# Kernel optimization log

Measured on AMD Instinct MI355X. Metric: run time of the kernel, lower is better.

Reference implementation:

```python
import jax, jax.numpy as jnp
import numpy as np

B_, L_, H_, N_ = 8, 1024, 1024, 64

def setup_inputs() -> dict:
    key = jax.random.key(0)
    k1, k2, k3, k4 = jax.random.split(key, 4)
    return {
        "samples": jax.random.normal(k1, (B_, L_, 3 * H_), dtype=jnp.float32),
        "label_one_hot": jax.random.uniform(k2, (B_, L_, N_), dtype=jnp.float32),
        "predict": jax.random.normal(k3, (B_, L_, N_), dtype=jnp.float32),
        "W": jax.random.normal(k4, (H_, 3 * H_), dtype=jnp.float32) * (1.0 / np.sqrt(3 * H_)),
        "b_proj": jnp.zeros((H_,), dtype=jnp.float32),
    }

def reference(samples, label_one_hot, predict, W, b_proj):
    # projection: Linear(3H -> H)
    s = jnp.einsum("blk,hk->blh", samples, W) + b_proj          # [b,L,H]
    # dense similarity graph with diagonal masked out, row-softmax
    graph = jnp.einsum("blh,bmh->blm", s, s)                     # [b,L,L]
    L = graph.shape[1]
    eye = jnp.eye(L, dtype=graph.dtype)
    A = jax.nn.softmax(graph - 1e5 * eye, axis=-1)               # [b,L,L]
    # centered masked labels
    sup = label_one_hot
    row_has = (jnp.sum(sup, axis=-1) > 0.5).astype(sup.dtype)    # [b,L]
    total = jnp.sum(row_has, axis=-1)[:, None]                   # [b,1]
    avg = (jnp.sum(sup, axis=-2) / total)[:, None, :]            # [b,1,N]
    B0 = (sup - avg) * row_has[..., None]                        # [b,L,N]
    # diagonal inverse-degree scaling (elementwise, no dense diag matmul)
    d = 1.0 / (jnp.sum(A, axis=-1) + 1e-10)                      # [b,L]
    P = d[:, :, None] * jnp.swapaxes(A, -1, -2)                  # [b,L,L]
    Db = d[:, :, None] * B0                                      # [b,L,N]
    # 6-step power-iteration scan with residual injection at t==3
    ut = jnp.zeros_like(B0)
    for t in range(1, 7):
        ut = jnp.einsum("blm,bmn->bln", P, ut) + Db
        if t == 3:
            ut = ut + predict  # dropout is identity in eval mode
    return ut

if __name__ == "__main__":
    out = reference(**setup_inputs())
    print(out.shape, out.dtype)
```

## Files before the change

kernel.cpp:

```cpp
#include <hip/hip_runtime.h>


typedef _Float16 f16_t;
typedef f16_t f16x4 __attribute__((ext_vector_type(4)));
typedef f16_t f16x8 __attribute__((ext_vector_type(8)));
typedef float floatx4 __attribute__((ext_vector_type(4)));

__device__ __forceinline__ void async_copy16(const void* g, void* l) {
  __builtin_amdgcn_global_load_lds(
      (const __attribute__((address_space(1))) void*)g,
      (__attribute__((address_space(3))) void*)l, 16, 0, 0);
}

__device__ __forceinline__ f16_t hi_of(float x) { return (f16_t)x; }
__device__ __forceinline__ f16_t lo_of(float x, f16_t h) {
  return (f16_t)(x - (float)h);
}

__global__ __launch_bounds__(256) void prep_kernel(
    const float* __restrict__ W, f16_t* __restrict__ Whi, f16_t* __restrict__ Wlo,
    const float* __restrict__ samples, f16_t* __restrict__ SampH)
{
  const int bx = blockIdx.x, tid = threadIdx.x;
  if (bx < 3072) {
    const int i = bx * 256 + tid;
    float4 v = ((const float4*)W)[i];
    v.x *= 32.f; v.y *= 32.f; v.z *= 32.f; v.w *= 32.f;
    f16x4 h, l;
    f16_t h0 = hi_of(v.x); h[0] = h0; l[0] = lo_of(v.x, h0);
    f16_t h1 = hi_of(v.y); h[1] = h1; l[1] = lo_of(v.y, h1);
    f16_t h2 = hi_of(v.z); h[2] = h2; l[2] = lo_of(v.z, h2);
    f16_t h3 = hi_of(v.w); h[3] = h3; l[3] = lo_of(v.w, h3);
    *(f16x4*)(Whi + (size_t)i * 4) = h;
    *(f16x4*)(Wlo + (size_t)i * 4) = l;
  } else {
    const int i = (bx - 3072) * 256 + tid;
    const float4 v = ((const float4*)samples)[i];
    f16x4 h;
    h[0] = (f16_t)v.x; h[1] = (f16_t)v.y; h[2] = (f16_t)v.z; h[3] = (f16_t)v.w;
    *(f16x4*)(SampH + (size_t)i * 4) = h;
  }
}

__global__ __launch_bounds__(512, 2) void gemm1_8ph(
    const f16_t* __restrict__ Ag,
    const f16_t* __restrict__ BhG, const f16_t* __restrict__ BlG,
    const float* __restrict__ bias,
    f16_t* __restrict__ Chi, f16_t* __restrict__ Clo,
    int N, int K, float cscale)
{
  __shared__ __align__(16) char smem[131072];

  const int tid = threadIdx.x;
  const int lane = tid & 63;
  const int wave = tid >> 6;
  const int wm = wave >> 2;
  const int wn = wave & 3;
  const int m0 = blockIdx.y * 256;
  const int n0 = blockIdx.x * 128;
  const int fr = lane & 15;
  const int lch = lane >> 4;

  const int gA0 = tid;
  const int gA1 = tid + 512;
  const int rA0 = gA0 >> 2, lcA0 = (gA0 & 3) ^ (rA0 & 3);
  const int rA1 = gA1 >> 2, lcA1 = (gA1 & 3) ^ (rA1 & 3);
  const int rB = tid >> 2, lcB = (tid & 3) ^ (rB & 3);
  const f16_t* aSrc0 = Ag + (size_t)(m0 + rA0) * K + lcA0 * 8;
  const f16_t* aSrc1 = Ag + (size_t)(m0 + rA1) * K + lcA1 * 8;
  const f16_t* bhSrc = BhG + (size_t)(n0 + rB) * K + lcB * 8;
  const f16_t* blSrc = BlG + (size_t)(n0 + rB) * K + lcB * 8;
  char* ldsA0 = smem + gA0 * 16;
  char* ldsA1 = smem + gA1 * 16;
  char* ldsBh = smem + 16384 + (size_t)tid * 16;
  char* ldsBl = smem + 24576 + (size_t)tid * 16;

  const int swz = ((lch ^ (fr & 3)) * 16);
  const int aoff = (wm * 128 + fr) * 64 + swz;
  const int boff = (wn * 32 + fr) * 64 + swz;

  floatx4 acc[8][2] = {};

#pragma unroll
  for (int s = 0; s < 3; ++s) {
    const int slot = s * 32768;
    const int k0 = s * 32;
    async_copy16(aSrc0 + k0, ldsA0 + slot);
    async_copy16(aSrc1 + k0, ldsA1 + slot);
    async_copy16(bhSrc + k0, ldsBh + slot);
    async_copy16(blSrc + k0, ldsBl + slot);
  }

  const int NS = K >> 5;
  for (int s = 0; s < NS; ++s) {
    asm volatile("s_waitcnt vmcnt(8)" ::: "memory");
    __builtin_amdgcn_s_barrier();

    const char* base = smem + (s & 3) * 32768;

    f16x8 bh0 = *(const f16x8*)(base + 16384 + boff);
    f16x8 bh1 = *(const f16x8*)(base + 16384 + boff + 1024);
    f16x8 bl0 = *(const f16x8*)(base + 24576 + boff);
    f16x8 bl1 = *(const f16x8*)(base + 24576 + boff + 1024);
    f16x8 a0[4];
#pragma unroll
    for (int i = 0; i < 4; ++i) a0[i] = *(const f16x8*)(base + aoff + i * 1024);

    {
      int ss = s + 3; if (ss >= NS) ss -= NS;
      const int slot = (ss & 3) * 32768;
      const int k0 = ss * 32;
      async_copy16(aSrc0 + k0, ldsA0 + slot);
      async_copy16(aSrc1 + k0, ldsA1 + slot);
      async_copy16(bhSrc + k0, ldsBh + slot);
      async_copy16(blSrc + k0, ldsBl + slot);
    }

    __builtin_amdgcn_s_setprio(1);
#pragma unroll
    for (int i = 0; i < 4; ++i) {
      acc[i][0] = __builtin_amdgcn_mfma_f32_16x16x32_f16(a0[i], bh0, acc[i][0], 0, 0, 0);
      acc[i][1] = __builtin_amdgcn_mfma_f32_16x16x32_f16(a0[i], bh1, acc[i][1], 0, 0, 0);
      acc[i][0] = __builtin_amdgcn_mfma_f32_16x16x32_f16(a0[i], bl0, acc[i][0], 0, 0, 0);
      acc[i][1] = __builtin_amdgcn_mfma_f32_16x16x32_f16(a0[i], bl1, acc[i][1], 0, 0, 0);
    }
    __builtin_amdgcn_s_setprio(0);

    f16x8 a1[4];
#pragma unroll
    for (int i = 0; i < 4; ++i) a1[i] = *(const f16x8*)(base + aoff + 4096 + i * 1024);

    __builtin_amdgcn_s_setprio(1);
#pragma unroll
    for (int i = 0; i < 4; ++i) {
      acc[i + 4][0] = __builtin_amdgcn_mfma_f32_16x16x32_f16(a1[i], bh0, acc[i + 4][0], 0, 0, 0);
      acc[i + 4][1] = __builtin_amdgcn_mfma_f32_16x16x32_f16(a1[i], bh1, acc[i + 4][1], 0, 0, 0);
      acc[i + 4][0] = __builtin_amdgcn_mfma_f32_16x16x32_f16(a1[i], bl0, acc[i + 4][0], 0, 0, 0);
      acc[i + 4][1] = __builtin_amdgcn_mfma_f32_16x16x32_f16(a1[i], bl1, acc[i + 4][1], 0, 0, 0);
    }
    __builtin_amdgcn_s_setprio(0);
  }
  asm volatile("s_waitcnt vmcnt(0)" ::: "memory");

  const int mr = (lane >> 4) * 4;
#pragma unroll
  for (int j = 0; j < 2; ++j) {
    const int n = n0 + wn * 32 + j * 16 + fr;
    const float bj = bias[n];
#pragma unroll
    for (int i = 0; i < 8; ++i) {
#pragma unroll
      for (int r = 0; r < 4; ++r) {
        const int m = m0 + wm * 128 + i * 16 + mr + r;
        float v = acc[i][j][r] * cscale + bj;
        f16_t h = hi_of(v);
        Chi[(size_t)m * N + n] = h;
        Clo[(size_t)m * N + n] = lo_of(v, h);
      }
    }
  }
}

template <int CMODE>
__global__ __launch_bounds__(256) void gemm_mfma(
    const f16_t* __restrict__ AhiG,
    const f16_t* __restrict__ BhiG, const f16_t* __restrict__ BloG,
    const float* __restrict__ bias,
    float* __restrict__ Cf, f16_t* __restrict__ Chi, f16_t* __restrict__ Clo,
    int M, int N, int K, long long sA, long long sB, long long sC, float cscale)
{
  AhiG += (long long)blockIdx.z * sA;
  BhiG += (long long)blockIdx.z * sB;
  BloG += (long long)blockIdx.z * sB;
  if (CMODE == 1) Cf += (long long)blockIdx.z * sC;

  __shared__ __align__(16) char smem[49152];
  f16_t* AsHi = (f16_t*)smem;
  f16_t* BsHi = (f16_t*)(smem + 16384);
  f16_t* BsLo = (f16_t*)(smem + 32768);

  const int tid = threadIdx.x;
  const int lane = tid & 63;
  const int wave = tid >> 6;
  const int wm = wave >> 1, wn = wave & 1;

  int m0, n0;
  if (CMODE == 0) {
    m0 = blockIdx.y * 128;
    n0 = blockIdx.x * 128;
  } else {
    int idx = blockIdx.x, i = 0, accu = 0;
    while (accu + i + 1 <= idx) { accu += i + 1; ++i; }
    m0 = i * 128;
    n0 = (idx - accu) * 128;
  }

  const int fr = lane & 15;
  const int kg = (lane >> 4) * 8;
  const int aoff = (wm * 64 + fr) * 32 + kg;
  const int boff = (wn * 64 + fr) * 32 + kg;

  floatx4 acc[4][4] = {};

  for (int k0 = 0; k0 < K; k0 += 64) {
    __syncthreads();
#pragma unroll
    for (int it = 0; it < 4; ++it) {
      const int cb = it * 256 + wave * 64;
      const int c = cb + lane;
      const int kk = c >> 9;
      const int row = (c >> 2) & 127;
      const int kc = kk * 32 + (c & 3) * 8;
      const size_t ga = (size_t)(m0 + row) * K + k0 + kc;
      const size_t gb = (size_t)(n0 + row) * K + k0 + kc;
      async_copy16(AhiG + ga, (char*)AsHi + (size_t)cb * 16);
      async_copy16(BhiG + gb, (char*)BsHi + (size_t)cb * 16);
      async_copy16(BloG + gb, (char*)BsLo + (size_t)cb * 16);
    }
    __syncthreads();

#pragma unroll
    for (int kk = 0; kk < 2; ++kk) {
      f16x8 ah[4], bh[4], bl[4];
#pragma unroll
      for (int t = 0; t < 4; ++t) {
        ah[t] = *(const f16x8*)&AsHi[kk * 4096 + aoff + t * 512];
        bh[t] = *(const f16x8*)&BsHi[kk * 4096 + boff + t * 512];
        bl[t] = *(const f16x8*)&BsLo[kk * 4096 + boff + t * 512];
      }
#pragma unroll
      for (int i = 0; i < 4; ++i)
#pragma unroll
        for (int j = 0; j < 4; ++j) {
          acc[i][j] = __builtin_amdgcn_mfma_f32_16x16x32_f16(ah[i], bh[j], acc[i][j], 0, 0, 0);
          acc[i][j] = __builtin_amdgcn_mfma_f32_16x16x32_f16(ah[i], bl[j], acc[i][j], 0, 0, 0);
        }
    }
  }

  const int mr = (lane >> 4) * 4;
#pragma unroll
  for (int j = 0; j < 4; ++j) {
    const int n = n0 + wn * 64 + j * 16 + fr;
    const float bj = (CMODE == 0) ? bias[n] : 0.f;
#pragma unroll
    for (int i = 0; i < 4; ++i) {
#pragma unroll
      for (int r = 0; r < 4; ++r) {
        const int m = m0 + wm * 64 + i * 16 + mr + r;
        float v = acc[i][j][r];
        if (CMODE == 0) {
          v = v * cscale + bj;
          f16_t h = hi_of(v);
          Chi[(size_t)m * N + n] = h;
          Clo[(size_t)m * N + n] = lo_of(v, h);
        } else {
          if (m == n) v -= 1e5f;
          Cf[(size_t)m * N + n] = v;
        }
      }
    }
  }

  if (CMODE == 1 && m0 != n0) {
    float* T = (float*)smem;
#pragma unroll
    for (int mc = 0; mc < 4; ++mc) {
      __syncthreads();
      if (wm == (mc >> 1)) {
        const int ibase = (mc & 1) * 2;
#pragma unroll
        for (int di = 0; di < 2; ++di) {
#pragma unroll
          for (int j = 0; j < 4; ++j) {
            const int nl = wn * 64 + j * 16 + fr;
#pragma unroll
            for (int r = 0; r < 4; ++r) {
              const int mloc = di * 16 + mr + r;
              T[nl * 36 + mloc] = acc[ibase + di][j][r];
            }
          }
        }
      }
      __syncthreads();
      const int row = tid >> 1, half = tid & 1;
      const float* src = &T[row * 36 + half * 16];
      float* dst = Cf + (size_t)(n0 + row) * N + m0 + mc * 32 + half * 16;
#pragma unroll
      for (int q = 0; q < 16; ++q) dst[q] = src[q];
    }
  }
}

__global__ __launch_bounds__(256) void rowstats_kernel(
    const float* __restrict__ G, float* __restrict__ mx, float* __restrict__ inv)
{
  __shared__ float red[4];
  const int tid = threadIdx.x;
  const float* g = G + (size_t)blockIdx.x * 1024;
  const float4 v = ((const float4*)g)[tid];

  float m = fmaxf(fmaxf(v.x, v.y), fmaxf(v.z, v.w));
#pragma unroll
  for (int off = 32; off > 0; off >>= 1) m = fmaxf(m, __shfl_down(m, off));
  if ((tid & 63) == 0) red[tid >> 6] = m;
  __syncthreads();
  m = fmaxf(fmaxf(red[0], red[1]), fmaxf(red[2], red[3]));
  __syncthreads();

  float s = __expf(v.x - m) + __expf(v.y - m) + __expf(v.z - m) + __expf(v.w - m);
#pragma unroll
  for (int off = 32; off > 0; off >>= 1) s += __shfl_down(s, off);
  if ((tid & 63) == 0) red[tid >> 6] = s;
  __syncthreads();
  if (tid == 0) {
    mx[blockIdx.x] = m;
    inv[blockIdx.x] = 1.0f / (red[0] + red[1] + red[2] + red[3]);
  }
}

__global__ __launch_bounds__(256) void make_at_kernel(
    const float* __restrict__ G, const float* __restrict__ mx,
    const float* __restrict__ inv, f16_t* __restrict__ At)
{
  const int row = blockIdx.x;
  const int b = row >> 10;
  const int tid = threadIdx.x;
  const float4 g = ((const float4*)(G + (size_t)row * 1024))[tid];
  const float4 m = ((const float4*)(mx + b * 1024))[tid];
  const float4 iv = ((const float4*)(inv + b * 1024))[tid];
  f16x4 o;
  o[0] = (f16_t)(__expf(g.x - m.x) * iv.x);
  o[1] = (f16_t)(__expf(g.y - m.y) * iv.y);
  o[2] = (f16_t)(__expf(g.z - m.z) * iv.z);
  o[3] = (f16_t)(__expf(g.w - m.w) * iv.w);
  *(f16x4*)(At + (size_t)row * 1024 + tid * 4) = o;
}

__global__ __launch_bounds__(1024) void make_db_kernel(
    const float* __restrict__ sup, float* __restrict__ Db, f16_t* __restrict__ DbT)
{
  const int L = 1024, Nn = 64;
  const float* s = sup + (size_t)blockIdx.x * L * Nn;
  float* db = Db + (size_t)blockIdx.x * L * Nn;
  f16_t* dbt = DbT + (size_t)blockIdx.x * L * Nn;
  __shared__ float rowhas[1024];
  __shared__ float cpart[1024];
  __shared__ float tpart[16];
  __shared__ float avg[64];
  __shared__ float totalsh;
  const int tid = threadIdx.x;

  const float4* sr = (const float4*)(s + (size_t)tid * 64);
  float ss = 0.f;
#pragma unroll
  for (int i = 0; i < 16; ++i) { const float4 v = sr[i]; ss += (v.x + v.y) + (v.z + v.w); }
  const float rh = (ss > 0.5f) ? 1.f : 0.f;
  rowhas[tid] = rh;
  float t = rh;
#pragma unroll
  for (int off = 32; off > 0; off >>= 1) t += __shfl_down(t, off);
  if ((tid & 63) == 0) tpart[tid >> 6] = t;

  const int n = tid & 63, seg = tid >> 6;
  float cs = 0.f;
  for (int l = seg * 64; l < seg * 64 + 64; ++l) cs += s[(size_t)l * 64 + n];
  cpart[seg * 64 + n] = cs;
  __syncthreads();
  if (tid == 0) { float tt = 0.f; for (int i = 0; i < 16; ++i) tt += tpart[i]; totalsh = tt; }
  __syncthreads();
  if (tid < 64) {
    float a = 0.f;
    for (int i = 0; i < 16; ++i) a += cpart[i * 64 + tid];
    avg[tid] = a / totalsh;
  }
  __syncthreads();

  const float4* s4 = (const float4*)s;
  float4* d4 = (float4*)db;
  for (int i = tid; i < (L * Nn) / 4; i += 1024) {
    float4 v = s4[i];
    const int l = i >> 4;
    const int nb = (i & 15) * 4;
    const float rhl = rowhas[l];
    v.x = (v.x - avg[nb + 0]) * rhl;
    v.y = (v.y - avg[nb + 1]) * rhl;
    v.z = (v.z - avg[nb + 2]) * rhl;
    v.w = (v.w - avg[nb + 3]) * rhl;
    d4[i] = v;
  }
  for (int i = tid; i < L * Nn; i += 1024) {
    const int n2 = i >> 10, l2 = i & 1023;
    dbt[i] = (f16_t)((s[(size_t)l2 * 64 + n2] - avg[n2]) * rowhas[l2]);
  }
}

__global__ __launch_bounds__(256) void iter_part(
    const f16_t* __restrict__ At, const f16_t* __restrict__ UT,
    float* __restrict__ Part)
{
  const int L = 1024, Nn = 64;
  const int b = blockIdx.y, l0 = blockIdx.x * 64, ks = blockIdx.z;
  At += (size_t)b * L * L;
  UT += (size_t)b * Nn * L;
  Part += (((size_t)ks * 8 + b) * L) * Nn;

  __shared__ __align__(16) f16_t AtS[2 * 64 * 32];
  __shared__ __align__(16) f16_t UtS[2 * 64 * 32];

  const int tid = threadIdx.x;
  const int lane = tid & 63;
  const int wave = tid >> 6;
  const int fr = lane & 15;
  const int kg = (lane >> 4) * 8;

  floatx4 acc[4] = {};

  for (int mi = 0; mi < 4; ++mi) {
    const int m0 = ks * 256 + mi * 64;
    __syncthreads();
#pragma unroll
    for (int it = 0; it < 2; ++it) {
      const int cb = it * 256 + wave * 64;
      const int c = cb + lane;
      const int kk = c >> 8;
      const int row = (c >> 2) & 63;
      const int kc = kk * 32 + (c & 3) * 8;
      async_copy16(At + (size_t)(l0 + row) * L + m0 + kc, (char*)AtS + (size_t)cb * 16);
      async_copy16(UT + (size_t)row * L + m0 + kc, (char*)UtS + (size_t)cb * 16);
    }
    __syncthreads();
#pragma unroll
    for (int kk = 0; kk < 2; ++kk) {
      const f16x8 a = *(const f16x8*)&AtS[kk * 2048 + (wave * 16 + fr) * 32 + kg];
#pragma unroll
      for (int j = 0; j < 4; ++j) {
        const f16x8 bf = *(const f16x8*)&UtS[kk * 2048 + (j * 16 + fr) * 32 + kg];
        acc[j] = __builtin_amdgcn_mfma_f32_16x16x32_f16(a, bf, acc[j], 0, 0, 0);
      }
    }
  }

  const int mr = (lane >> 4) * 4;
#pragma unroll
  for (int j = 0; j < 4; ++j) {
    const int n = j * 16 + fr;
#pragma unroll
    for (int r = 0; r < 4; ++r) {
      const int l = wave * 16 + mr + r;
      Part[(size_t)(l0 + l) * Nn + n] = acc[j][r];
    }
  }
}

template <int PRED, int FINAL>
__global__ __launch_bounds__(256) void iter_fin(
    const float* __restrict__ Part, const float* __restrict__ Db,
    const float* __restrict__ Pred, f16_t* __restrict__ UTn,
    float* __restrict__ OutF)
{
  const int L = 1024, Nn = 64;
  const int b = blockIdx.y, l0 = blockIdx.x * 64;
  const size_t base = ((size_t)b * L + l0) * Nn;
  const size_t ksStride = (size_t)8 * L * Nn;
  Db += base;
  if (PRED) Pred += base;

  __shared__ f16_t OutS[64 * 72];
  const int tid = threadIdx.x;

#pragma unroll
  for (int it = 0; it < 4; ++it) {
    const int idx = it * 256 + tid;
    const int l = idx >> 4, n4 = (idx & 15) * 4;
    const size_t o = (size_t)l * Nn + n4;
    float4 v = *(const float4*)(Part + base + o);
    const float4 p1 = *(const float4*)(Part + base + ksStride + o);
    const float4 p2 = *(const float4*)(Part + base + 2 * ksStride + o);
    const float4 p3 = *(const float4*)(Part + base + 3 * ksStride + o);
    v.x += p1.x; v.y += p1.y; v.z += p1.z; v.w += p1.w;
    v.x += p2.x; v.y += p2.y; v.z += p2.z; v.w += p2.w;
    v.x += p3.x; v.y += p3.y; v.z += p3.z; v.w += p3.w;
    const float4 d = *(const float4*)(Db + o);
    v.x += d.x; v.y += d.y; v.z += d.z; v.w += d.w;
    if (PRED) {
      const float4 p = *(const float4*)(Pred + o);
      v.x += p.x; v.y += p.y; v.z += p.z; v.w += p.w;
    }
    if (FINAL) {
      *(float4*)(OutF + base + o) = v;
    } else {
      OutS[(n4 + 0) * 72 + l] = (f16_t)v.x;
      OutS[(n4 + 1) * 72 + l] = (f16_t)v.y;
      OutS[(n4 + 2) * 72 + l] = (f16_t)v.z;
      OutS[(n4 + 3) * 72 + l] = (f16_t)v.w;
    }
  }
  if (!FINAL) {
    __syncthreads();
    f16_t* dst = UTn + (size_t)b * Nn * L;
#pragma unroll
    for (int it = 0; it < 2; ++it) {
      const int c = it * 256 + tid;
      const int n = c >> 3, lc = (c & 7) * 8;
      *(f16x8*)(dst + (size_t)n * L + l0 + lc) = *(const f16x8*)&OutS[n * 72 + lc];
    }
  }
}

extern "C" void kernel_launch(void* const* d_in, const int* in_sizes, int n_in,
                              void* d_out, int out_size, void* d_ws, size_t ws_size,
                              hipStream_t stream) {
  const float* samples = (const float*)d_in[0];
  const float* label   = (const float*)d_in[1];
  const float* predict = (const float*)d_in[2];
  const float* W       = (const float*)d_in[3];
  const float* bproj   = (const float*)d_in[4];
  float* out = (float*)d_out;

  char* ws = (char*)d_ws;
  f16_t* Whi = (f16_t*)ws;
  f16_t* Wlo = (f16_t*)(ws + 6291456);
  float* mx  = (float*)ws;
  float* inv = (float*)(ws + 32768);
  float* Db  = (float*)(ws + 65536);
  f16_t* DbT = (f16_t*)(ws + 65536 + 2097152);
  f16_t* UTa = (f16_t*)(ws + 65536 + 3145728);
  f16_t* UTb = (f16_t*)(ws + 65536 + 4194304);
  f16_t* SampH = (f16_t*)(ws + 12582912);
  float* G     = (float*)(ws + 12582912);
  f16_t* Shi = (f16_t*)(ws + 62914560);
  f16_t* Slo = (f16_t*)(ws + 62914560 + 16777216);
  f16_t* At  = Shi;
  float* Part = (float*)Slo;

  const long long LH = 1024LL * 1024;
  const long long LL = 1024LL * 1024;

  prep_kernel<<<dim3(27648), 256, 0, stream>>>(W, Whi, Wlo, samples, SampH);

  gemm1_8ph<<<dim3(8, 32), 512, 0, stream>>>(
      SampH, Whi, Wlo, bproj, Shi, Slo, 1024, 3072, 1.0f / 32.0f);

  gemm_mfma<1><<<dim3(36, 1, 8), 256, 0, stream>>>(
      Shi, Shi, Slo, nullptr, G, nullptr, nullptr,
      1024, 1024, 1024, LH, LH, LL, 1.0f);

  rowstats_kernel<<<8192, 256, 0, stream>>>(G, mx, inv);
  make_at_kernel<<<8192, 256, 0, stream>>>(G, mx, inv, At);

  make_db_kernel<<<8, 1024, 0, stream>>>(label, Db, DbT);

  dim3 gp(16, 8, 4), gf(16, 8);
  iter_part<<<gp, 256, 0, stream>>>(At, DbT, Part);
  iter_fin<0, 0><<<gf, 256, 0, stream>>>(Part, Db, nullptr, UTa, nullptr);
  iter_part<<<gp, 256, 0, stream>>>(At, UTa, Part);
  iter_fin<1, 0><<<gf, 256, 0, stream>>>(Part, Db, predict, UTb, nullptr);
  iter_part<<<gp, 256, 0, stream>>>(At, UTb, Part);
  iter_fin<0, 0><<<gf, 256, 0, stream>>>(Part, Db, nullptr, UTa, nullptr);
  iter_part<<<gp, 256, 0, stream>>>(At, UTa, Part);
  iter_fin<0, 0><<<gf, 256, 0, stream>>>(Part, Db, nullptr, UTb, nullptr);
  iter_part<<<gp, 256, 0, stream>>>(At, UTb, Part);
  iter_fin<0, 1><<<gf, 256, 0, stream>>>(Part, Db, nullptr, nullptr, out);
}
```

Baseline: 407.8 us.

## Double-buffer LDS fragment loads in projection GEMM and change swizzle pattern

```diff
diff --git a/kernel.cpp b/kernel.cpp
--- a/kernel.cpp
+++ b/kernel.cpp
@@ -42,7 +42,38 @@
   }
 }
 
-__global__ __launch_bounds__(512, 2) void gemm1_8ph(
+struct Frags {
+  f16x8 a[8];
+  f16x8 bh0, bh1, bl0, bl1;
+};
+
+__device__ __forceinline__ void load_frags(const char* base, int aoff, int boff,
+                                           Frags& f) {
+  f.bh0 = *(const f16x8*)(base + 16384 + boff);
+  f.bh1 = *(const f16x8*)(base + 16384 + boff + 1024);
+  f.bl0 = *(const f16x8*)(base + 24576 + boff);
+  f.bl1 = *(const f16x8*)(base + 24576 + boff + 1024);
+#pragma unroll
+  for (int i = 0; i < 8; ++i)
+    f.a[i] = *(const f16x8*)(base + aoff + i * 1024);
+}
+
+__device__ __forceinline__ void mfma_all(const Frags& f, floatx4 acc[8][2]) {
+  __builtin_amdgcn_s_setprio(1);
+#pragma unroll
+  for (int i = 0; i < 8; ++i) {
+    acc[i][0] = __builtin_amdgcn_mfma_f32_16x16x32_f16(f.a[i], f.bh0, acc[i][0], 0, 0, 0);
+    acc[i][1] = __builtin_amdgcn_mfma_f32_16x16x32_f16(f.a[i], f.bh1, acc[i][1], 0, 0, 0);
+  }
+#pragma unroll
+  for (int i = 0; i < 8; ++i) {
+    acc[i][0] = __builtin_amdgcn_mfma_f32_16x16x32_f16(f.a[i], f.bl0, acc[i][0], 0, 0, 0);
+    acc[i][1] = __builtin_amdgcn_mfma_f32_16x16x32_f16(f.a[i], f.bl1, acc[i][1], 0, 0, 0);
+  }
+  __builtin_amdgcn_s_setprio(0);
+}
+
+__global__ __launch_bounds__(512, 2) void gemm1_pipe(
     const f16_t* __restrict__ Ag,
     const f16_t* __restrict__ BhG, const f16_t* __restrict__ BlG,
     const float* __restrict__ bias,
@@ -63,9 +94,9 @@
 
   const int gA0 = tid;
   const int gA1 = tid + 512;
-  const int rA0 = gA0 >> 2, lcA0 = (gA0 & 3) ^ (rA0 & 3);
-  const int rA1 = gA1 >> 2, lcA1 = (gA1 & 3) ^ (rA1 & 3);
-  const int rB = tid >> 2, lcB = (tid & 3) ^ (rB & 3);
+  const int rA0 = gA0 >> 2, lcA0 = (gA0 & 3) ^ ((rA0 >> 1) & 3);
+  const int rA1 = gA1 >> 2, lcA1 = (gA1 & 3) ^ ((rA1 >> 1) & 3);
+  const int rB = tid >> 2, lcB = (tid & 3) ^ ((rB >> 1) & 3);
   const f16_t* aSrc0 = Ag + (size_t)(m0 + rA0) * K + lcA0 * 8;
   const f16_t* aSrc1 = Ag + (size_t)(m0 + rA1) * K + lcA1 * 8;
   const f16_t* bhSrc = BhG + (size_t)(n0 + rB) * K + lcB * 8;
@@ -75,72 +106,48 @@
   char* ldsBh = smem + 16384 + (size_t)tid * 16;
   char* ldsBl = smem + 24576 + (size_t)tid * 16;
 
-  const int swz = ((lch ^ (fr & 3)) * 16);
+  const int swz = (lch ^ ((fr >> 1) & 3)) * 16;
   const int aoff = (wm * 128 + fr) * 64 + swz;
   const int boff = (wn * 32 + fr) * 64 + swz;
 
   floatx4 acc[8][2] = {};
-
-#pragma unroll
-  for (int s = 0; s < 3; ++s) {
-    const int slot = s * 32768;
-    const int k0 = s * 32;
-    async_copy16(aSrc0 + k0, ldsA0 + slot);
-    async_copy16(aSrc1 + k0, ldsA1 + slot);
-    async_copy16(bhSrc + k0, ldsBh + slot);
-    async_copy16(blSrc + k0, ldsBl + slot);
-  }
-
   const int NS = K >> 5;
-  for (int s = 0; s < NS; ++s) {
+
+#define STAGE(SS_)                                            \
+  do {                                                        \
+    int ss = (SS_); if (ss >= NS) ss -= NS;                   \
+    const int slot = (ss & 3) * 32768;                        \
+    const int k0 = ss * 32;                                   \
+    async_copy16(aSrc0 + k0, ldsA0 + slot);                   \
+    async_copy16(aSrc1 + k0, ldsA1 + slot);                   \
+    async_copy16(bhSrc + k0, ldsBh + slot);                   \
+    async_copy16(blSrc + k0, ldsBl + slot);                   \
+  } while (0)
+
+  Frags f0, f1;
+
+  STAGE(0); STAGE(1); STAGE(2);
+  asm volatile("s_waitcnt vmcnt(8)" ::: "memory");
+  __builtin_amdgcn_s_barrier();
+  load_frags(smem, aoff, boff, f0);
+
+  for (int s = 0; s < NS; s += 2) {
+    STAGE(s + 3);
     asm volatile("s_waitcnt vmcnt(8)" ::: "memory");
+    asm volatile("s_waitcnt lgkmcnt(0)" ::: "memory");
     __builtin_amdgcn_s_barrier();
-
-    const char* base = smem + (s & 3) * 32768;
-
-    f16x8 bh0 = *(const f16x8*)(base + 16384 + boff);
-    f16x8 bh1 = *(const f16x8*)(base + 16384 + boff + 1024);
-    f16x8 bl0 = *(const f16x8*)(base + 24576 + boff);
-    f16x8 bl1 = *(const f16x8*)(base + 24576 + boff + 1024);
-    f16x8 a0[4];
-#pragma unroll
-    for (int i = 0; i < 4; ++i) a0[i] = *(const f16x8*)(base + aoff + i * 1024);
-
-    {
-      int ss = s + 3; if (ss >= NS) ss -= NS;
-      const int slot = (ss & 3) * 32768;
-      const int k0 = ss * 32;
-      async_copy16(aSrc0 + k0, ldsA0 + slot);
-      async_copy16(aSrc1 + k0, ldsA1 + slot);
-      async_copy16(bhSrc + k0, ldsBh + slot);
-      async_copy16(blSrc + k0, ldsBl + slot);
-    }
-
-    __builtin_amdgcn_s_setprio(1);
-#pragma unroll
-    for (int i = 0; i < 4; ++i) {
-      acc[i][0] = __builtin_amdgcn_mfma_f32_16x16x32_f16(a0[i], bh0, acc[i][0], 0, 0, 0);
-      acc[i][1] = __builtin_amdgcn_mfma_f32_16x16x32_f16(a0[i], bh1, acc[i][1], 0, 0, 0);
-      acc[i][0] = __builtin_amdgcn_mfma_f32_16x16x32_f16(a0[i], bl0, acc[i][0], 0, 0, 0);
-      acc[i][1] = __builtin_amdgcn_mfma_f32_16x16x32_f16(a0[i], bl1, acc[i][1], 0, 0, 0);
-    }
-    __builtin_amdgcn_s_setprio(0);
-
-    f16x8 a1[4];
-#pragma unroll
-    for (int i = 0; i < 4; ++i) a1[i] = *(const f16x8*)(base + aoff + 4096 + i * 1024);
-
-    __builtin_amdgcn_s_setprio(1);
-#pragma unroll
-    for (int i = 0; i < 4; ++i) {
-      acc[i + 4][0] = __builtin_amdgcn_mfma_f32_16x16x32_f16(a1[i], bh0, acc[i + 4][0], 0, 0, 0);
-      acc[i + 4][1] = __builtin_amdgcn_mfma_f32_16x16x32_f16(a1[i], bh1, acc[i + 4][1], 0, 0, 0);
-      acc[i + 4][0] = __builtin_amdgcn_mfma_f32_16x16x32_f16(a1[i], bl0, acc[i + 4][0], 0, 0, 0);
-      acc[i + 4][1] = __builtin_amdgcn_mfma_f32_16x16x32_f16(a1[i], bl1, acc[i + 4][1], 0, 0, 0);
-    }
-    __builtin_amdgcn_s_setprio(0);
+    load_frags(smem + ((s + 1) & 3) * 32768, aoff, boff, f1);
+    mfma_all(f0, acc);
+
+    STAGE(s + 4);
+    asm volatile("s_waitcnt vmcnt(8)" ::: "memory");
+    asm volatile("s_waitcnt lgkmcnt(0)" ::: "memory");
+    __builtin_amdgcn_s_barrier();
+    load_frags(smem + ((s + 2) & 3) * 32768, aoff, boff, f0);
+    mfma_all(f1, acc);
   }
   asm volatile("s_waitcnt vmcnt(0)" ::: "memory");
+#undef STAGE
 
   const int mr = (lane >> 4) * 4;
 #pragma unroll
@@ -539,7 +546,7 @@
 
   prep_kernel<<<dim3(27648), 256, 0, stream>>>(W, Whi, Wlo, samples, SampH);
 
-  gemm1_8ph<<<dim3(8, 32), 512, 0, stream>>>(
+  gemm1_pipe<<<dim3(8, 32), 512, 0, stream>>>(
       SampH, Whi, Wlo, bproj, Shi, Slo, 1024, 3072, 1.0f / 32.0f);
 
   gemm_mfma<1><<<dim3(36, 1, 8), 256, 0, stream>>>(
```

After: 406.0 us. No clear change (-0.4%).
